# Kernel optimization log

Measured on AMD Instinct MI355X. Metric: run time of the kernel, lower is better.

## Reference

```python
import jax, jax.numpy as jnp
import numpy as np

TEMP = 10.0      # ZCA_temp -> diagonal regularizer 1/temp on the covariance
T_ITERS = 10     # ZCA_iteration: Newton-Schulz steps


def newton_zca(h, temp=TEMP, T=T_ITERS):
    """Newton-Schulz ZCA whitening of features h: [N, D].
    Returns (whitened [N,D], mean [1,D], whitening matrix C [D,D])."""
    n = h.shape[0]
    d = h.shape[1]
    mean = jnp.mean(h, axis=0, keepdims=True)            # [1, D]
    xc = h - mean                                        # [N, D]
    I = jnp.eye(d, dtype=h.dtype)
    cov = (xc.T @ xc) / n + I / temp                     # [D, D]
    tr = jnp.trace(cov)
    S = cov / tr                                         # spectral-normalized cov

    def step(P, _):
        # P <- 0.5 * (3 P - P^3 S)
        P = 1.5 * P - 0.5 * (P @ P @ (P @ S))
        return P, None

    P, _ = jax.lax.scan(step, I, None, length=T)
    C = P / jnp.sqrt(tr)                                 # cov^{-1/2}
    return xc @ C, mean, C


def setup_inputs() -> dict:
    key = jax.random.key(0)
    kx, k0, k1, k2 = jax.random.split(key, 4)
    N, DIN, D = 65536, 512, 512

    def glorot(k, din, dout):
        lim = jnp.sqrt(6.0 / (din + dout)).astype(jnp.float32)
        return jax.random.uniform(k, (din, dout), jnp.float32, -lim, lim)

    return {
        "x": jax.random.normal(kx, (N, DIN), jnp.float32),
        "W0": glorot(k0, DIN, D),
        "W1": glorot(k1, D, D),
        "W2": glorot(k2, D, D),
    }


def reference(x, W0, W1, W2):
    # training=True path, activation = identity, dropout rate 0.0 (identity).
    h0, _, _ = newton_zca(x @ W0)    # dense 0 + ZCA
    h1, _, _ = newton_zca(h0 @ W1)   # dense 1 + ZCA
    h2, _, _ = newton_zca(h1 @ W2)   # output dense + ZCA
    # deep_copy_list of per-layer activations
    return (h0, h1, h2)
```

## Files before the change

### kernel.cpp

```cpp
#include <hip/hip_runtime.h>

#define NROWS 65536
#define DIM   512
#define INV_N (1.0f/65536.0f)
#define INV_TEMP 0.1f
#define T_ITERS 10

__global__ __launch_bounds__(256) void colsum_part_k(const float* __restrict__ in,
                                                     float* __restrict__ part) {
    int ch = blockIdx.x;
    int t  = threadIdx.x;
    int c  = 2 * t;
    const float* p = in + (size_t)ch * 1024 * DIM + c;
    float s0 = 0.f, s1 = 0.f;
    for (int r = 0; r < 1024; ++r) {
        float2 v = *reinterpret_cast<const float2*>(p + (size_t)r * DIM);
        s0 += v.x; s1 += v.y;
    }
    part[ch * DIM + c]     = s0;
    part[ch * DIM + c + 1] = s1;
}

__global__ __launch_bounds__(256) void gram_k(const float* __restrict__ in,
                                              float* __restrict__ gp) {
    __shared__ float As[16][68];
    __shared__ float Bs[16][68];
    int ci0 = blockIdx.x * 64, cj0 = blockIdx.y * 64;
    int z = blockIdx.z;
    int t = threadIdx.x;
    int tx = t & 15, ty = t >> 4;
    int lr = t >> 4;
    int lc = (t & 15) * 4;
    float acc[4][4] = {};
    const float* baseA = in + (size_t)z * 4096 * DIM;
    const float* pa = baseA + (size_t)lr * DIM + ci0 + lc;
    const float* pb = baseA + (size_t)lr * DIM + cj0 + lc;
    float4 a = *reinterpret_cast<const float4*>(pa);
    float4 b = *reinterpret_cast<const float4*>(pb);
    for (int k0 = 0; k0 < 4096; k0 += 16) {
        __syncthreads();
        *reinterpret_cast<float4*>(&As[lr][lc]) = a;
        *reinterpret_cast<float4*>(&Bs[lr][lc]) = b;
        __syncthreads();
        if (k0 + 16 < 4096) {
            a = *reinterpret_cast<const float4*>(pa + (size_t)(k0 + 16) * DIM);
            b = *reinterpret_cast<const float4*>(pb + (size_t)(k0 + 16) * DIM);
        }
#pragma unroll
        for (int k = 0; k < 16; ++k) {
            float4 av = *reinterpret_cast<const float4*>(&As[k][4 * ty]);
            float4 bv = *reinterpret_cast<const float4*>(&Bs[k][4 * tx]);
            float aa[4] = {av.x, av.y, av.z, av.w};
            float bb[4] = {bv.x, bv.y, bv.z, bv.w};
#pragma unroll
            for (int i = 0; i < 4; ++i)
#pragma unroll
                for (int j = 0; j < 4; ++j)
                    acc[i][j] = fmaf(aa[i], bb[j], acc[i][j]);
        }
    }
    float* o = gp + (size_t)z * DIM * DIM;
#pragma unroll
    for (int i = 0; i < 4; ++i) {
        float4 v = {acc[i][0], acc[i][1], acc[i][2], acc[i][3]};
        *reinterpret_cast<float4*>(o + (size_t)(ci0 + 4 * ty + i) * DIM + cj0 + 4 * tx) = v;
    }
}

__global__ __launch_bounds__(256) void gram_reduce_k(const float* __restrict__ gp,
                                                     float* __restrict__ G) {
    int idx = (blockIdx.x * 256 + threadIdx.x) * 4;
    float4 s = {0.f, 0.f, 0.f, 0.f};
    for (int ch = 0; ch < 16; ++ch) {
        float4 v = *reinterpret_cast<const float4*>(gp + (size_t)ch * DIM * DIM + idx);
        s.x += v.x; s.y += v.y; s.z += v.z; s.w += v.w;
    }
    *reinterpret_cast<float4*>(G + idx) = s;
}

__global__ __launch_bounds__(256) void meanh_k(const float* __restrict__ part,
                                               const float* __restrict__ W,
                                               float* __restrict__ mh) {
    __shared__ float cs[DIM];
    int t = threadIdx.x;
    for (int c = t; c < DIM; c += 256) {
        float s = 0.f;
        for (int ch = 0; ch < 64; ++ch) s += part[ch * DIM + c];
        cs[c] = s;
    }
    __syncthreads();
    for (int c = t; c < DIM; c += 256) {
        float s = 0.f;
        for (int k = 0; k < DIM; ++k) s = fmaf(cs[k], W[(size_t)k * DIM + c], s);
        mh[c] = s * INV_N;
    }
}

__device__ __forceinline__ void small_gemm_body(const float* __restrict__ A, int ta,
                                                const float* __restrict__ B,
                                                float* __restrict__ C, int mode,
                                                const float* __restrict__ scal, int sidx,
                                                int bx, int by) {
    __shared__ float As[32][36];
    __shared__ float Bs[32][36];
    int m0 = bx * 32, n0 = by * 32;
    int t = threadIdx.x;
    int tx = t & 15, ty = t >> 4;
    int lr = t >> 3;
    int lc = (t & 7) * 4;
    float acc[2][2] = {};
    float4 av, bv;
    if (ta) av = *reinterpret_cast<const float4*>(A + (size_t)lr * DIM + m0 + lc);
    else    av = *reinterpret_cast<const float4*>(A + (size_t)(m0 + lr) * DIM + lc);
    bv = *reinterpret_cast<const float4*>(B + (size_t)lr * DIM + n0 + lc);
    for (int k0 = 0; k0 < DIM; k0 += 32) {
        __syncthreads();
        if (ta) {
            *reinterpret_cast<float4*>(&As[lr][lc]) = av;
        } else {
            As[lc + 0][lr] = av.x; As[lc + 1][lr] = av.y;
            As[lc + 2][lr] = av.z; As[lc + 3][lr] = av.w;
        }
        *reinterpret_cast<float4*>(&Bs[lr][lc]) = bv;
        __syncthreads();
        if (k0 + 32 < DIM) {
            if (ta) av = *reinterpret_cast<const float4*>(A + (size_t)(k0 + 32 + lr) * DIM + m0 + lc);
            else    av = *reinterpret_cast<const float4*>(A + (size_t)(m0 + lr) * DIM + k0 + 32 + lc);
            bv = *reinterpret_cast<const float4*>(B + (size_t)(k0 + 32 + lr) * DIM + n0 + lc);
        }
#pragma unroll
        for (int k = 0; k < 32; ++k) {
            float a0 = As[k][2 * ty], a1 = As[k][2 * ty + 1];
            float b0 = Bs[k][2 * tx], b1 = Bs[k][2 * tx + 1];
            acc[0][0] = fmaf(a0, b0, acc[0][0]);
            acc[0][1] = fmaf(a0, b1, acc[0][1]);
            acc[1][0] = fmaf(a1, b0, acc[1][0]);
            acc[1][1] = fmaf(a1, b1, acc[1][1]);
        }
    }
    int m = m0 + 2 * ty, nn = n0 + 2 * tx;
    size_t i00 = (size_t)m * DIM + nn, i10 = (size_t)(m + 1) * DIM + nn;
    if (mode == 0) {
        C[i00] = acc[0][0]; C[i00 + 1] = acc[0][1];
        C[i10] = acc[1][0]; C[i10 + 1] = acc[1][1];
    } else if (mode == 1) {
        C[i00]     = 1.5f * C[i00]     - 0.5f * acc[0][0];
        C[i00 + 1] = 1.5f * C[i00 + 1] - 0.5f * acc[0][1];
        C[i10]     = 1.5f * C[i10]     - 0.5f * acc[1][0];
        C[i10 + 1] = 1.5f * C[i10 + 1] - 0.5f * acc[1][1];
    } else {
        float s = scal[sidx];
        C[i00] = acc[0][0] * s; C[i00 + 1] = acc[0][1] * s;
        C[i10] = acc[1][0] * s; C[i10 + 1] = acc[1][1] * s;
    }
}

__global__ __launch_bounds__(256) void small_gemm_k(const float* __restrict__ A, int ta,
                                                    const float* __restrict__ B,
                                                    float* __restrict__ C, int mode,
                                                    const float* __restrict__ scal, int sidx) {
    small_gemm_body(A, ta, B, C, mode, scal, sidx, blockIdx.x, blockIdx.y);
}

__global__ __launch_bounds__(256) void ns_tt_k(const float* __restrict__ P,
                                               const float* __restrict__ S,
                                               float* __restrict__ T1,
                                               float* __restrict__ T2) {
    if (blockIdx.z == 0) small_gemm_body(P, 0, P, T1, 0, nullptr, 0, blockIdx.x, blockIdx.y);
    else                 small_gemm_body(P, 0, S, T2, 0, nullptr, 0, blockIdx.x, blockIdx.y);
}

__global__ __launch_bounds__(256) void trace_k(const float* __restrict__ covh,
                                               const float* __restrict__ mh,
                                               float* __restrict__ scal) {
    __shared__ float red[256];
    int t = threadIdx.x;
    float s = 0.f;
    for (int i = t; i < DIM; i += 256)
        s += covh[(size_t)i * DIM + i] * INV_N - mh[i] * mh[i] + INV_TEMP;
    red[t] = s;
    __syncthreads();
    for (int o = 128; o > 0; o >>= 1) {
        if (t < o) red[t] += red[t + o];
        __syncthreads();
    }
    if (t == 0) {
        float tr = red[0];
        scal[0] = 1.0f / tr;
        scal[1] = 1.0f / sqrtf(tr);
    }
}

__global__ __launch_bounds__(256) void makeS_k(const float* __restrict__ covh,
                                               const float* __restrict__ mh,
                                               const float* __restrict__ scal,
                                               float* __restrict__ S) {
    int idx = blockIdx.x * 256 + threadIdx.x;
    int i = idx >> 9, j = idx & 511;
    float v = covh[idx] * INV_N - mh[i] * mh[j] + ((i == j) ? INV_TEMP : 0.f);
    S[idx] = v * scal[0];
}

__global__ __launch_bounds__(256) void initP_k(float* __restrict__ P) {
    int idx = blockIdx.x * 256 + threadIdx.x;
    int i = idx >> 9, j = idx & 511;
    P[idx] = (i == j) ? 1.0f : 0.f;
}

__global__ __launch_bounds__(256) void bias_k(const float* __restrict__ mh,
                                              const float* __restrict__ P,
                                              const float* __restrict__ scal,
                                              float* __restrict__ bias) {
    __shared__ float m_s[DIM];
    int t = threadIdx.x;
    for (int c = t; c < DIM; c += 256) m_s[c] = mh[c];
    __syncthreads();
    float ist = scal[1];
    for (int c = t; c < DIM; c += 256) {
        float s = 0.f;
        for (int k = 0; k < DIM; ++k) s = fmaf(m_s[k], P[(size_t)k * DIM + c], s);
        bias[c] = s * ist;
    }
}

__global__ __launch_bounds__(256) void out_gemm_k(const float* __restrict__ in,
                                                  const float* __restrict__ WC,
                                                  const float* __restrict__ bias,
                                                  float* __restrict__ out) {
    __shared__ float As[16][68];
    __shared__ float Bs[16][68];
    int n0 = blockIdx.x * 64, m0 = blockIdx.y * 64;
    int t = threadIdx.x;
    int tx = t & 15, ty = t >> 4;
    int ar = t >> 2;
    int ac = (t & 3) * 4;
    int br = t >> 4;
    int bc = (t & 15) * 4;
    float acc[4][4] = {};
    const float* pa = in + (size_t)(m0 + ar) * DIM + ac;
    const float* pb = WC + (size_t)br * DIM + n0 + bc;
    float4 a = *reinterpret_cast<const float4*>(pa);
    float4 b = *reinterpret_cast<const float4*>(pb);
    for (int k0 = 0; k0 < DIM; k0 += 16) {
        __syncthreads();
        As[ac + 0][ar] = a.x; As[ac + 1][ar] = a.y;
        As[ac + 2][ar] = a.z; As[ac + 3][ar] = a.w;
        *reinterpret_cast<float4*>(&Bs[br][bc]) = b;
        __syncthreads();
        if (k0 + 16 < DIM) {
            a = *reinterpret_cast<const float4*>(pa + k0 + 16);
            b = *reinterpret_cast<const float4*>(pb + (size_t)(k0 + 16) * DIM);
        }
#pragma unroll
        for (int k = 0; k < 16; ++k) {
            float4 av = *reinterpret_cast<const float4*>(&As[k][4 * ty]);
            float4 bv = *reinterpret_cast<const float4*>(&Bs[k][4 * tx]);
            float aa[4] = {av.x, av.y, av.z, av.w};
            float bb[4] = {bv.x, bv.y, bv.z, bv.w};
#pragma unroll
            for (int i = 0; i < 4; ++i)
#pragma unroll
                for (int j = 0; j < 4; ++j)
                    acc[i][j] = fmaf(aa[i], bb[j], acc[i][j]);
        }
    }
    float4 bvv = *reinterpret_cast<const float4*>(bias + n0 + 4 * tx);
    float bb[4] = {bvv.x, bvv.y, bvv.z, bvv.w};
#pragma unroll
    for (int i = 0; i < 4; ++i) {
        float4 v = {acc[i][0] - bb[0], acc[i][1] - bb[1],
                    acc[i][2] - bb[2], acc[i][3] - bb[3]};
        *reinterpret_cast<float4*>(out + (size_t)(m0 + 4 * ty + i) * DIM + n0 + 4 * tx) = v;
    }
}

extern "C" void kernel_launch(void* const* d_in, const int* in_sizes, int n_in,
                              void* d_out, int out_size, void* d_ws, size_t ws_size,
                              hipStream_t stream) {
    const float* x = (const float*)d_in[0];
    const float* Wl[3] = {(const float*)d_in[1], (const float*)d_in[2], (const float*)d_in[3]};
    float* out = (float*)d_out;
    float* ws  = (float*)d_ws;

    const size_t MM = (size_t)DIM * DIM;
    float* G     = ws;
    float* S     = G + MM;
    float* P     = S + MM;
    float* T1    = P + MM;
    float* T2    = T1 + MM;
    float* covh  = T2 + MM;
    float* WC    = covh + MM;
    float* gramp = WC + MM;
    float* cpart = gramp + 16 * MM;
    float* mh    = cpart + 64 * DIM;
    float* bias  = mh + DIM;
    float* scal  = bias + DIM;

    for (int l = 0; l < 3; ++l) {
        const float* in = (l == 0) ? x : out + (size_t)(l - 1) * NROWS * DIM;
        const float* W  = Wl[l];
        float* o = out + (size_t)l * NROWS * DIM;

        colsum_part_k<<<64, 256, 0, stream>>>(in, cpart);
        gram_k<<<dim3(8, 8, 16), 256, 0, stream>>>(in, gramp);
        gram_reduce_k<<<256, 256, 0, stream>>>(gramp, G);
        meanh_k<<<1, 256, 0, stream>>>(cpart, W, mh);
        small_gemm_k<<<dim3(16, 16), 256, 0, stream>>>(G, 0, W, T1, 0, nullptr, 0);
        small_gemm_k<<<dim3(16, 16), 256, 0, stream>>>(W, 1, T1, covh, 0, nullptr, 0);
        trace_k<<<1, 256, 0, stream>>>(covh, mh, scal);
        makeS_k<<<1024, 256, 0, stream>>>(covh, mh, scal, S);
        initP_k<<<1024, 256, 0, stream>>>(P);
        for (int it = 0; it < T_ITERS; ++it) {
            ns_tt_k<<<dim3(16, 16, 2), 256, 0, stream>>>(P, S, T1, T2);
            small_gemm_k<<<dim3(16, 16), 256, 0, stream>>>(T1, 0, T2, P, 1, nullptr, 0);
        }
        small_gemm_k<<<dim3(16, 16), 256, 0, stream>>>(W, 0, P, WC, 2, scal, 1);
        bias_k<<<1, 256, 0, stream>>>(mh, P, scal, bias);
        out_gemm_k<<<dim3(8, 1024), 256, 0, stream>>>(in, WC, bias, o);
    }
}
```

Baseline: 4.952 ms.

## Rewrite ZCA pipeline with split-bf16 MFMA gemms and cooperative Newton-Schulz kernel

The Gram matrix and output GEMMs now run on MFMA bf16 instructions with a hi/lo split (three products) to approximate fp32 accuracy. The Gram is computed only for upper-triangular tiles, accumulated with atomics, and fused with the column sum. The small-matrix chain (covariance, trace, Newton-Schulz iterations, WC and bias) moves into one cooperative kernel with grid syncs instead of dozens of launches, with a multi-kernel fallback. The costs are reduced precision from the bf16 split, atomic contention, and dependence on cooperative launch support.

```diff
diff --git a/kernel.cpp b/kernel.cpp
--- a/kernel.cpp
+++ b/kernel.cpp
@@ -1,4 +1,7 @@
 #include <hip/hip_runtime.h>
+#include <hip/hip_cooperative_groups.h>
+
+namespace cg = cooperative_groups;
 
 #define NROWS 65536
 #define DIM   512
@@ -6,113 +9,162 @@
 #define INV_TEMP 0.1f
 #define T_ITERS 10
 
-__global__ __launch_bounds__(256) void colsum_part_k(const float* __restrict__ in,
-                                                     float* __restrict__ part) {
-    int ch = blockIdx.x;
-    int t  = threadIdx.x;
-    int c  = 2 * t;
-    const float* p = in + (size_t)ch * 1024 * DIM + c;
-    float s0 = 0.f, s1 = 0.f;
-    for (int r = 0; r < 1024; ++r) {
-        float2 v = *reinterpret_cast<const float2*>(p + (size_t)r * DIM);
-        s0 += v.x; s1 += v.y;
-    }
-    part[ch * DIM + c]     = s0;
-    part[ch * DIM + c + 1] = s1;
-}
-
-__global__ __launch_bounds__(256) void gram_k(const float* __restrict__ in,
-                                              float* __restrict__ gp) {
-    __shared__ float As[16][68];
-    __shared__ float Bs[16][68];
-    int ci0 = blockIdx.x * 64, cj0 = blockIdx.y * 64;
-    int z = blockIdx.z;
+typedef __attribute__((ext_vector_type(8))) short bf16x8;
+typedef __attribute__((ext_vector_type(4))) float f32x4;
+
+#define OFF_G    0
+#define OFF_SCAL 262144
+#define OFF_CS   262208
+#define OFF_S    262720
+#define OFF_P    (OFF_S  + 262144)
+#define OFF_T1   (OFF_P  + 262144)
+#define OFF_T2   (OFF_T1 + 262144)
+#define OFF_CV   (OFF_T2 + 262144)
+#define OFF_MH   (OFF_CV + 262144)
+#define OFF_BIAS (OFF_MH + 512)
+#define OFF_WCH  (OFF_BIAS + 512)
+#define OFF_WCL  (OFF_WCH + 131072)
+
+__device__ __forceinline__ unsigned short bf_hi(float x) {
+    return (unsigned short)(__float_as_uint(x) >> 16);
+}
+__device__ __forceinline__ float bf_f(unsigned short h) {
+    return __uint_as_float(((unsigned)h) << 16);
+}
+
+__global__ __launch_bounds__(256) void zero_k(float* __restrict__ ws) {
+    int idx = blockIdx.x * 256 + threadIdx.x;
+    if (idx < 65680) reinterpret_cast<float4*>(ws)[idx] = make_float4(0.f, 0.f, 0.f, 0.f);
+}
+
+__global__ __launch_bounds__(256, 2) void gram_k(const float* __restrict__ in,
+                                                 float* __restrict__ G,
+                                                 float* __restrict__ cs) {
+    __shared__ unsigned short Ah[128][40], Al[128][40], Bh[128][40], Bl[128][40];
+    int u = blockIdx.x, z = blockIdx.y;
+    int bi, bj;
+    if (u < 4)      { bi = 0; bj = u; }
+    else if (u < 7) { bi = 1; bj = u - 3; }
+    else if (u < 9) { bi = 2; bj = u - 5; }
+    else            { bi = 3; bj = 3; }
+    bool diag = (bi == bj);
+    int ci0 = bi * 128, cj0 = bj * 128;
+    int t = threadIdx.x;
+    int d = t & 127, nh = (t >> 7) * 16;
+    const float* baseA = in + (size_t)z * 2048 * DIM + ci0 + d;
+    const float* baseB = in + (size_t)z * 2048 * DIM + cj0 + d;
+    int lane = t & 63, w = t >> 6;
+    int wr = (w >> 1) * 64, wc = (w & 1) * 64;
+    int fr = lane & 15, kg = lane >> 4;
+    f32x4 acc[4][4];
+#pragma unroll
+    for (int i = 0; i < 4; ++i)
+#pragma unroll
+        for (int j = 0; j < 4; ++j) acc[i][j] = (f32x4){0.f, 0.f, 0.f, 0.f};
+    float pA[16], pB[16];
+    float csum = 0.f;
+#pragma unroll
+    for (int j = 0; j < 16; ++j) pA[j] = baseA[(size_t)(nh + j) * DIM];
+    if (!diag) {
+#pragma unroll
+        for (int j = 0; j < 16; ++j) pB[j] = baseB[(size_t)(nh + j) * DIM];
+    }
+    for (int s = 0; s < 64; ++s) {
+        __syncthreads();
+        if (diag) {
+#pragma unroll
+            for (int j = 0; j < 16; ++j) csum += pA[j];
+        }
+#pragma unroll
+        for (int gq = 0; gq < 2; ++gq) {
+            unsigned hw[4], lw[4];
+#pragma unroll
+            for (int q = 0; q < 4; ++q) {
+                float x0 = pA[gq * 8 + 2 * q], x1 = pA[gq * 8 + 2 * q + 1];
+                unsigned short h0 = bf_hi(x0), h1 = bf_hi(x1);
+                unsigned short l0 = bf_hi(x0 - bf_f(h0)), l1 = bf_hi(x1 - bf_f(h1));
+                hw[q] = (unsigned)h0 | ((unsigned)h1 << 16);
+                lw[q] = (unsigned)l0 | ((unsigned)l1 << 16);
+            }
+            *reinterpret_cast<uint4*>(&Ah[d][nh + 8 * gq]) = make_uint4(hw[0], hw[1], hw[2], hw[3]);
+            *reinterpret_cast<uint4*>(&Al[d][nh + 8 * gq]) = make_uint4(lw[0], lw[1], lw[2], lw[3]);
+        }
+        if (!diag) {
+#pragma unroll
+            for (int gq = 0; gq < 2; ++gq) {
+                unsigned hw[4], lw[4];
+#pragma unroll
+                for (int q = 0; q < 4; ++q) {
+                    float x0 = pB[gq * 8 + 2 * q], x1 = pB[gq * 8 + 2 * q + 1];
+                    unsigned short h0 = bf_hi(x0), h1 = bf_hi(x1);
+                    unsigned short l0 = bf_hi(x0 - bf_f(h0)), l1 = bf_hi(x1 - bf_f(h1));
+                    hw[q] = (unsigned)h0 | ((unsigned)h1 << 16);
+                    lw[q] = (unsigned)l0 | ((unsigned)l1 << 16);
+                }
+                *reinterpret_cast<uint4*>(&Bh[d][nh + 8 * gq]) = make_uint4(hw[0], hw[1], hw[2], hw[3]);
+                *reinterpret_cast<uint4*>(&Bl[d][nh + 8 * gq]) = make_uint4(lw[0], lw[1], lw[2], lw[3]);
+            }
+        }
+        __syncthreads();
+        if (s + 1 < 64) {
+#pragma unroll
+            for (int j = 0; j < 16; ++j)
+                pA[j] = baseA[(size_t)((s + 1) * 32 + nh + j) * DIM];
+            if (!diag) {
+#pragma unroll
+                for (int j = 0; j < 16; ++j)
+                    pB[j] = baseB[(size_t)((s + 1) * 32 + nh + j) * DIM];
+            }
+        }
+        const unsigned short (*pBh)[40] = diag ? Ah : Bh;
+        const unsigned short (*pBl)[40] = diag ? Al : Bl;
+        bf16x8 ah[4], al4[4], bh4[4], bl4[4];
+#pragma unroll
+        for (int f = 0; f < 4; ++f) {
+            ah[f]  = *reinterpret_cast<const bf16x8*>(&Ah[wr + f * 16 + fr][kg * 8]);
+            al4[f] = *reinterpret_cast<const bf16x8*>(&Al[wr + f * 16 + fr][kg * 8]);
+            bh4[f] = *reinterpret_cast<const bf16x8*>(&pBh[wc + f * 16 + fr][kg * 8]);
+            bl4[f] = *reinterpret_cast<const bf16x8*>(&pBl[wc + f * 16 + fr][kg * 8]);
+        }
+#pragma unroll
+        for (int i = 0; i < 4; ++i)
+#pragma unroll
+            for (int j = 0; j < 4; ++j) {
+                f32x4 c = acc[i][j];
+                c = __builtin_amdgcn_mfma_f32_16x16x32_bf16(ah[i],  bh4[j], c, 0, 0, 0);
+                c = __builtin_amdgcn_mfma_f32_16x16x32_bf16(ah[i],  bl4[j], c, 0, 0, 0);
+                c = __builtin_amdgcn_mfma_f32_16x16x32_bf16(al4[i], bh4[j], c, 0, 0, 0);
+                acc[i][j] = c;
+            }
+    }
+#pragma unroll
+    for (int i = 0; i < 4; ++i) {
+        int row = ci0 + wr + i * 16 + kg * 4;
+#pragma unroll
+        for (int j = 0; j < 4; ++j) {
+            int col = cj0 + wc + j * 16 + fr;
+#pragma unroll
+            for (int r = 0; r < 4; ++r)
+                atomicAdd(&G[(size_t)(row + r) * DIM + col], acc[i][j][r]);
+        }
+    }
+    if (diag) atomicAdd(&cs[ci0 + d], csum);
+}
+
+__device__ void gemm_tile(const float* __restrict__ A, int ta,
+                          const float* __restrict__ B,
+                          float* C, int tile, int mode, float* ws) {
+    __shared__ float As[32][36];
+    __shared__ float Bs[32][36];
+    int m0 = (tile >> 4) * 32, n0 = (tile & 15) * 32;
     int t = threadIdx.x;
     int tx = t & 15, ty = t >> 4;
-    int lr = t >> 4;
-    int lc = (t & 15) * 4;
-    float acc[4][4] = {};
-    const float* baseA = in + (size_t)z * 4096 * DIM;
-    const float* pa = baseA + (size_t)lr * DIM + ci0 + lc;
-    const float* pb = baseA + (size_t)lr * DIM + cj0 + lc;
-    float4 a = *reinterpret_cast<const float4*>(pa);
-    float4 b = *reinterpret_cast<const float4*>(pb);
-    for (int k0 = 0; k0 < 4096; k0 += 16) {
-        __syncthreads();
-        *reinterpret_cast<float4*>(&As[lr][lc]) = a;
-        *reinterpret_cast<float4*>(&Bs[lr][lc]) = b;
-        __syncthreads();
-        if (k0 + 16 < 4096) {
-            a = *reinterpret_cast<const float4*>(pa + (size_t)(k0 + 16) * DIM);
-            b = *reinterpret_cast<const float4*>(pb + (size_t)(k0 + 16) * DIM);
-        }
-#pragma unroll
-        for (int k = 0; k < 16; ++k) {
-            float4 av = *reinterpret_cast<const float4*>(&As[k][4 * ty]);
-            float4 bv = *reinterpret_cast<const float4*>(&Bs[k][4 * tx]);
-            float aa[4] = {av.x, av.y, av.z, av.w};
-            float bb[4] = {bv.x, bv.y, bv.z, bv.w};
-#pragma unroll
-            for (int i = 0; i < 4; ++i)
-#pragma unroll
-                for (int j = 0; j < 4; ++j)
-                    acc[i][j] = fmaf(aa[i], bb[j], acc[i][j]);
-        }
-    }
-    float* o = gp + (size_t)z * DIM * DIM;
-#pragma unroll
-    for (int i = 0; i < 4; ++i) {
-        float4 v = {acc[i][0], acc[i][1], acc[i][2], acc[i][3]};
-        *reinterpret_cast<float4*>(o + (size_t)(ci0 + 4 * ty + i) * DIM + cj0 + 4 * tx) = v;
-    }
-}
-
-__global__ __launch_bounds__(256) void gram_reduce_k(const float* __restrict__ gp,
-                                                     float* __restrict__ G) {
-    int idx = (blockIdx.x * 256 + threadIdx.x) * 4;
-    float4 s = {0.f, 0.f, 0.f, 0.f};
-    for (int ch = 0; ch < 16; ++ch) {
-        float4 v = *reinterpret_cast<const float4*>(gp + (size_t)ch * DIM * DIM + idx);
-        s.x += v.x; s.y += v.y; s.z += v.z; s.w += v.w;
-    }
-    *reinterpret_cast<float4*>(G + idx) = s;
-}
-
-__global__ __launch_bounds__(256) void meanh_k(const float* __restrict__ part,
-                                               const float* __restrict__ W,
-                                               float* __restrict__ mh) {
-    __shared__ float cs[DIM];
-    int t = threadIdx.x;
-    for (int c = t; c < DIM; c += 256) {
-        float s = 0.f;
-        for (int ch = 0; ch < 64; ++ch) s += part[ch * DIM + c];
-        cs[c] = s;
-    }
-    __syncthreads();
-    for (int c = t; c < DIM; c += 256) {
-        float s = 0.f;
-        for (int k = 0; k < DIM; ++k) s = fmaf(cs[k], W[(size_t)k * DIM + c], s);
-        mh[c] = s * INV_N;
-    }
-}
-
-__device__ __forceinline__ void small_gemm_body(const float* __restrict__ A, int ta,
-                                                const float* __restrict__ B,
-                                                float* __restrict__ C, int mode,
-                                                const float* __restrict__ scal, int sidx,
-                                                int bx, int by) {
-    __shared__ float As[32][36];
-    __shared__ float Bs[32][36];
-    int m0 = bx * 32, n0 = by * 32;
-    int t = threadIdx.x;
-    int tx = t & 15, ty = t >> 4;
-    int lr = t >> 3;
-    int lc = (t & 7) * 4;
-    float acc[2][2] = {};
+    int lr = t >> 3, lc = (t & 7) * 4;
+    float acc00 = 0.f, acc01 = 0.f, acc10 = 0.f, acc11 = 0.f;
     float4 av, bv;
-    if (ta) av = *reinterpret_cast<const float4*>(A + (size_t)lr * DIM + m0 + lc);
-    else    av = *reinterpret_cast<const float4*>(A + (size_t)(m0 + lr) * DIM + lc);
-    bv = *reinterpret_cast<const float4*>(B + (size_t)lr * DIM + n0 + lc);
+    av = ta ? *reinterpret_cast<const float4*>(&A[(size_t)lr * DIM + m0 + lc])
+            : *reinterpret_cast<const float4*>(&A[(size_t)(m0 + lr) * DIM + lc]);
+    bv = *reinterpret_cast<const float4*>(&B[(size_t)lr * DIM + n0 + lc]);
     for (int k0 = 0; k0 < DIM; k0 += 32) {
         __syncthreads();
         if (ta) {
@@ -124,198 +176,299 @@
         *reinterpret_cast<float4*>(&Bs[lr][lc]) = bv;
         __syncthreads();
         if (k0 + 32 < DIM) {
-            if (ta) av = *reinterpret_cast<const float4*>(A + (size_t)(k0 + 32 + lr) * DIM + m0 + lc);
-            else    av = *reinterpret_cast<const float4*>(A + (size_t)(m0 + lr) * DIM + k0 + 32 + lc);
-            bv = *reinterpret_cast<const float4*>(B + (size_t)(k0 + 32 + lr) * DIM + n0 + lc);
+            av = ta ? *reinterpret_cast<const float4*>(&A[(size_t)(k0 + 32 + lr) * DIM + m0 + lc])
+                    : *reinterpret_cast<const float4*>(&A[(size_t)(m0 + lr) * DIM + k0 + 32 + lc]);
+            bv = *reinterpret_cast<const float4*>(&B[(size_t)(k0 + 32 + lr) * DIM + n0 + lc]);
         }
 #pragma unroll
         for (int k = 0; k < 32; ++k) {
             float a0 = As[k][2 * ty], a1 = As[k][2 * ty + 1];
             float b0 = Bs[k][2 * tx], b1 = Bs[k][2 * tx + 1];
-            acc[0][0] = fmaf(a0, b0, acc[0][0]);
-            acc[0][1] = fmaf(a0, b1, acc[0][1]);
-            acc[1][0] = fmaf(a1, b0, acc[1][0]);
-            acc[1][1] = fmaf(a1, b1, acc[1][1]);
-        }
-    }
-    int m = m0 + 2 * ty, nn = n0 + 2 * tx;
-    size_t i00 = (size_t)m * DIM + nn, i10 = (size_t)(m + 1) * DIM + nn;
+            acc00 = fmaf(a0, b0, acc00); acc01 = fmaf(a0, b1, acc01);
+            acc10 = fmaf(a1, b0, acc10); acc11 = fmaf(a1, b1, acc11);
+        }
+    }
+    int m = m0 + 2 * ty, n = n0 + 2 * tx;
+    size_t i00 = (size_t)m * DIM + n, i10 = (size_t)(m + 1) * DIM + n;
     if (mode == 0) {
-        C[i00] = acc[0][0]; C[i00 + 1] = acc[0][1];
-        C[i10] = acc[1][0]; C[i10 + 1] = acc[1][1];
+        C[i00] = acc00; C[i00 + 1] = acc01; C[i10] = acc10; C[i10 + 1] = acc11;
     } else if (mode == 1) {
-        C[i00]     = 1.5f * C[i00]     - 0.5f * acc[0][0];
-        C[i00 + 1] = 1.5f * C[i00 + 1] - 0.5f * acc[0][1];
-        C[i10]     = 1.5f * C[i10]     - 0.5f * acc[1][0];
-        C[i10 + 1] = 1.5f * C[i10 + 1] - 0.5f * acc[1][1];
+        C[i00]     = 1.5f * C[i00]     - 0.5f * acc00;
+        C[i00 + 1] = 1.5f * C[i00 + 1] - 0.5f * acc01;
+        C[i10]     = 1.5f * C[i10]     - 0.5f * acc10;
+        C[i10 + 1] = 1.5f * C[i10 + 1] - 0.5f * acc11;
+    } else if (mode == 2) {
+        C[i00] = acc00; C[i00 + 1] = acc01; C[i10] = acc10; C[i10 + 1] = acc11;
+        if (m == n) atomicAdd(ws + OFF_SCAL, (acc00 + acc11) * INV_N);
     } else {
-        float s = scal[sidx];
-        C[i00] = acc[0][0] * s; C[i00 + 1] = acc[0][1] * s;
-        C[i10] = acc[1][0] * s; C[i10 + 1] = acc[1][1] * s;
-    }
-}
-
-__global__ __launch_bounds__(256) void small_gemm_k(const float* __restrict__ A, int ta,
-                                                    const float* __restrict__ B,
-                                                    float* __restrict__ C, int mode,
-                                                    const float* __restrict__ scal, int sidx) {
-    small_gemm_body(A, ta, B, C, mode, scal, sidx, blockIdx.x, blockIdx.y);
-}
-
-__global__ __launch_bounds__(256) void ns_tt_k(const float* __restrict__ P,
-                                               const float* __restrict__ S,
-                                               float* __restrict__ T1,
-                                               float* __restrict__ T2) {
-    if (blockIdx.z == 0) small_gemm_body(P, 0, P, T1, 0, nullptr, 0, blockIdx.x, blockIdx.y);
-    else                 small_gemm_body(P, 0, S, T2, 0, nullptr, 0, blockIdx.x, blockIdx.y);
-}
-
-__global__ __launch_bounds__(256) void trace_k(const float* __restrict__ covh,
-                                               const float* __restrict__ mh,
-                                               float* __restrict__ scal) {
+        unsigned short* WCth = (unsigned short*)(ws + OFF_WCH);
+        unsigned short* WCtl = (unsigned short*)(ws + OFF_WCL);
+        float istr = 1.0f / sqrtf(ws[OFF_SCAL]);
+        float v;
+        unsigned short h;
+        v = acc00 * istr; h = bf_hi(v);
+        WCth[(size_t)n * DIM + m] = h;           WCtl[(size_t)n * DIM + m] = bf_hi(v - bf_f(h));
+        v = acc01 * istr; h = bf_hi(v);
+        WCth[(size_t)(n + 1) * DIM + m] = h;     WCtl[(size_t)(n + 1) * DIM + m] = bf_hi(v - bf_f(h));
+        v = acc10 * istr; h = bf_hi(v);
+        WCth[(size_t)n * DIM + m + 1] = h;       WCtl[(size_t)n * DIM + m + 1] = bf_hi(v - bf_f(h));
+        v = acc11 * istr; h = bf_hi(v);
+        WCth[(size_t)(n + 1) * DIM + m + 1] = h; WCtl[(size_t)(n + 1) * DIM + m + 1] = bf_hi(v - bf_f(h));
+    }
+}
+
+__global__ __launch_bounds__(256) void coop_k(float* ws, const float* __restrict__ W) {
+    cg::grid_group g = cg::this_grid();
+    float* G  = ws + OFF_G;   float* scal = ws + OFF_SCAL;
+    float* cs = ws + OFF_CS;  float* S    = ws + OFF_S;
+    float* P  = ws + OFF_P;   float* T1   = ws + OFF_T1;
+    float* T2 = ws + OFF_T2;  float* CV   = ws + OFF_CV;
+    float* mh = ws + OFF_MH;  float* bias = ws + OFF_BIAS;
+    int b = blockIdx.x, t = threadIdx.x;
+    int gtid = b * 256 + t;
+#pragma unroll
+    for (int e = 0; e < 4; ++e) {
+        int idx = gtid * 4 + e;
+        int i = idx >> 9, j = idx & 511;
+        if (i < j) G[(size_t)j * DIM + i] = G[idx];
+    }
+    g.sync();
+    gemm_tile(G, 0, W, T1, b, 0, ws);
+    if (b == 0) {
+        for (int c = t; c < DIM; c += 256) {
+            float s = 0.f;
+            for (int k = 0; k < DIM; ++k) s = fmaf(cs[k], W[(size_t)k * DIM + c], s);
+            mh[c] = s * INV_N;
+        }
+    }
+    g.sync();
+    gemm_tile(W, 1, T1, CV, b, 2, ws);
+    if (b == 0) {
+        __shared__ float red[256];
+        red[t] = mh[t] * mh[t] + mh[t + 256] * mh[t + 256];
+        __syncthreads();
+        for (int o = 128; o > 0; o >>= 1) { if (t < o) red[t] += red[t + o]; __syncthreads(); }
+        if (t == 0) atomicAdd(scal, 51.2f - red[0]);
+    }
+    g.sync();
+    {
+        float invtr = 1.0f / scal[0];
+#pragma unroll
+        for (int e = 0; e < 4; ++e) {
+            int idx = gtid * 4 + e;
+            int i = idx >> 9, j = idx & 511;
+            float v = CV[idx] * INV_N - mh[i] * mh[j] + ((i == j) ? INV_TEMP : 0.f);
+            S[idx] = v * invtr;
+            P[idx] = (i == j) ? 1.f : 0.f;
+        }
+    }
+    g.sync();
+    for (int it = 0; it < T_ITERS; ++it) {
+        gemm_tile(P, 0, P, T1, b, 0, ws);
+        gemm_tile(P, 0, S, T2, b, 0, ws);
+        g.sync();
+        gemm_tile(T1, 0, T2, P, b, 1, ws);
+        g.sync();
+    }
+    gemm_tile(W, 0, P, nullptr, b, 3, ws);
+    if (b == 0) {
+        float istr = 1.0f / sqrtf(scal[0]);
+        for (int c = t; c < DIM; c += 256) {
+            float s = 0.f;
+            for (int k = 0; k < DIM; ++k) s = fmaf(mh[k], P[(size_t)k * DIM + c], s);
+            bias[c] = s * istr;
+        }
+    }
+}
+
+__global__ __launch_bounds__(256, 2) void out_k(const float* __restrict__ in,
+                                                const unsigned short* __restrict__ WCth,
+                                                const unsigned short* __restrict__ WCtl,
+                                                const float* __restrict__ bias,
+                                                float* __restrict__ out) {
+    __shared__ unsigned short Ah[128][72], Al[128][72], Bh[128][72], Bl[128][72];
+    int n0 = blockIdx.x * 128, m0 = blockIdx.y * 128;
+    int t = threadIdx.x;
+    int lane = t & 63, w = t >> 6;
+    int wr = (w >> 1) * 64, wc = (w & 1) * 64;
+    int fr = lane & 15, kg = lane >> 4;
+    int am = t >> 4, aq = (t & 15) * 4;
+    int bn = t >> 3, bc = (t & 7) * 8;
+    f32x4 acc[4][4];
+#pragma unroll
+    for (int i = 0; i < 4; ++i)
+#pragma unroll
+        for (int j = 0; j < 4; ++j) acc[i][j] = (f32x4){0.f, 0.f, 0.f, 0.f};
+    float4 pa[8]; uint4 pbh[4], pbl[4];
+#pragma unroll
+    for (int p = 0; p < 8; ++p)
+        pa[p] = *reinterpret_cast<const float4*>(&in[(size_t)(m0 + p * 16 + am) * DIM + aq]);
+#pragma unroll
+    for (int p = 0; p < 4; ++p) {
+        pbh[p] = *reinterpret_cast<const uint4*>(&WCth[(size_t)(n0 + p * 32 + bn) * DIM + bc]);
+        pbl[p] = *reinterpret_cast<const uint4*>(&WCtl[(size_t)(n0 + p * 32 + bn) * DIM + bc]);
+    }
+    for (int s = 0; s < 8; ++s) {
+        __syncthreads();
+#pragma unroll
+        for (int p = 0; p < 8; ++p) {
+            float4 v = pa[p];
+            unsigned short h0 = bf_hi(v.x), h1 = bf_hi(v.y), h2 = bf_hi(v.z), h3 = bf_hi(v.w);
+            unsigned short l0 = bf_hi(v.x - bf_f(h0)), l1 = bf_hi(v.y - bf_f(h1));
+            unsigned short l2 = bf_hi(v.z - bf_f(h2)), l3 = bf_hi(v.w - bf_f(h3));
+            *reinterpret_cast<uint2*>(&Ah[p * 16 + am][aq]) =
+                make_uint2((unsigned)h0 | ((unsigned)h1 << 16), (unsigned)h2 | ((unsigned)h3 << 16));
+            *reinterpret_cast<uint2*>(&Al[p * 16 + am][aq]) =
+                make_uint2((unsigned)l0 | ((unsigned)l1 << 16), (unsigned)l2 | ((unsigned)l3 << 16));
+        }
+#pragma unroll
+        for (int p = 0; p < 4; ++p) {
+            *reinterpret_cast<uint4*>(&Bh[p * 32 + bn][bc]) = pbh[p];
+            *reinterpret_cast<uint4*>(&Bl[p * 32 + bn][bc]) = pbl[p];
+        }
+        __syncthreads();
+        if (s + 1 < 8) {
+            int k0 = (s + 1) * 64;
+#pragma unroll
+            for (int p = 0; p < 8; ++p)
+                pa[p] = *reinterpret_cast<const float4*>(&in[(size_t)(m0 + p * 16 + am) * DIM + k0 + aq]);
+#pragma unroll
+            for (int p = 0; p < 4; ++p) {
+                pbh[p] = *reinterpret_cast<const uint4*>(&WCth[(size_t)(n0 + p * 32 + bn) * DIM + k0 + bc]);
+                pbl[p] = *reinterpret_cast<const uint4*>(&WCtl[(size_t)(n0 + p * 32 + bn) * DIM + k0 + bc]);
+            }
+        }
+#pragma unroll
+        for (int k2 = 0; k2 < 2; ++k2) {
+            int ko = k2 * 32 + kg * 8;
+            bf16x8 ah[4], al4[4], bh4[4], bl4[4];
+#pragma unroll
+            for (int f = 0; f < 4; ++f) {
+                ah[f]  = *reinterpret_cast<const bf16x8*>(&Ah[wr + f * 16 + fr][ko]);
+                al4[f] = *reinterpret_cast<const bf16x8*>(&Al[wr + f * 16 + fr][ko]);
+                bh4[f] = *reinterpret_cast<const bf16x8*>(&Bh[wc + f * 16 + fr][ko]);
+                bl4[f] = *reinterpret_cast<const bf16x8*>(&Bl[wc + f * 16 + fr][ko]);
+            }
+#pragma unroll
+            for (int i = 0; i < 4; ++i)
+#pragma unroll
+                for (int j = 0; j < 4; ++j) {
+                    f32x4 c = acc[i][j];
+                    c = __builtin_amdgcn_mfma_f32_16x16x32_bf16(ah[i],  bh4[j], c, 0, 0, 0);
+                    c = __builtin_amdgcn_mfma_f32_16x16x32_bf16(ah[i],  bl4[j], c, 0, 0, 0);
+                    c = __builtin_amdgcn_mfma_f32_16x16x32_bf16(al4[i], bh4[j], c, 0, 0, 0);
+                    acc[i][j] = c;
+                }
+        }
+    }
+#pragma unroll
+    for (int j = 0; j < 4; ++j) {
+        int col = n0 + wc + j * 16 + fr;
+        float bb = bias[col];
+#pragma unroll
+        for (int i = 0; i < 4; ++i) {
+            int row = m0 + wr + i * 16 + kg * 4;
+#pragma unroll
+            for (int r = 0; r < 4; ++r)
+                out[(size_t)(row + r) * DIM + col] = acc[i][j][r] - bb;
+        }
+    }
+}
+
+__global__ __launch_bounds__(256) void tile_gemm_k(const float* __restrict__ A, int ta,
+                                                   const float* __restrict__ B,
+                                                   float* C, int mode, float* ws) {
+    gemm_tile(A, ta, B, C, blockIdx.x, mode, ws);
+}
+__global__ __launch_bounds__(256) void mirror_k(float* ws) {
+    float* G = ws + OFF_G;
+    int gtid = blockIdx.x * 256 + threadIdx.x;
+#pragma unroll
+    for (int e = 0; e < 4; ++e) {
+        int idx = gtid * 4 + e;
+        int i = idx >> 9, j = idx & 511;
+        if (i < j) G[(size_t)j * DIM + i] = G[idx];
+    }
+}
+__global__ __launch_bounds__(256) void mh_k(float* ws, const float* __restrict__ W) {
+    float* cs = ws + OFF_CS; float* mh = ws + OFF_MH;
+    int c = blockIdx.x * 256 + threadIdx.x;
+    float s = 0.f;
+    for (int k = 0; k < DIM; ++k) s = fmaf(cs[k], W[(size_t)k * DIM + c], s);
+    mh[c] = s * INV_N;
+}
+__global__ __launch_bounds__(256) void trmh_k(float* ws) {
     __shared__ float red[256];
+    float* mh = ws + OFF_MH;
     int t = threadIdx.x;
+    red[t] = mh[t] * mh[t] + mh[t + 256] * mh[t + 256];
+    __syncthreads();
+    for (int o = 128; o > 0; o >>= 1) { if (t < o) red[t] += red[t + o]; __syncthreads(); }
+    if (t == 0) atomicAdd(ws + OFF_SCAL, 51.2f - red[0]);
+}
+__global__ __launch_bounds__(256) void makeSP_k(float* ws) {
+    float* CV = ws + OFF_CV; float* mh = ws + OFF_MH;
+    float* S = ws + OFF_S;   float* P = ws + OFF_P;
+    float invtr = 1.0f / ws[OFF_SCAL];
+    int gtid = blockIdx.x * 256 + threadIdx.x;
+#pragma unroll
+    for (int e = 0; e < 4; ++e) {
+        int idx = gtid * 4 + e;
+        int i = idx >> 9, j = idx & 511;
+        float v = CV[idx] * INV_N - mh[i] * mh[j] + ((i == j) ? INV_TEMP : 0.f);
+        S[idx] = v * invtr;
+        P[idx] = (i == j) ? 1.f : 0.f;
+    }
+}
+__global__ __launch_bounds__(256) void bias_k(float* ws) {
+    float* mh = ws + OFF_MH; float* P = ws + OFF_P; float* bias = ws + OFF_BIAS;
+    float istr = 1.0f / sqrtf(ws[OFF_SCAL]);
+    int c = blockIdx.x * 256 + threadIdx.x;
     float s = 0.f;
-    for (int i = t; i < DIM; i += 256)
-        s += covh[(size_t)i * DIM + i] * INV_N - mh[i] * mh[i] + INV_TEMP;
-    red[t] = s;
-    __syncthreads();
-    for (int o = 128; o > 0; o >>= 1) {
-        if (t < o) red[t] += red[t + o];
-        __syncthreads();
-    }
-    if (t == 0) {
-        float tr = red[0];
-        scal[0] = 1.0f / tr;
-        scal[1] = 1.0f / sqrtf(tr);
-    }
-}
-
-__global__ __launch_bounds__(256) void makeS_k(const float* __restrict__ covh,
-                                               const float* __restrict__ mh,
-                                               const float* __restrict__ scal,
-                                               float* __restrict__ S) {
-    int idx = blockIdx.x * 256 + threadIdx.x;
-    int i = idx >> 9, j = idx & 511;
-    float v = covh[idx] * INV_N - mh[i] * mh[j] + ((i == j) ? INV_TEMP : 0.f);
-    S[idx] = v * scal[0];
-}
-
-__global__ __launch_bounds__(256) void initP_k(float* __restrict__ P) {
-    int idx = blockIdx.x * 256 + threadIdx.x;
-    int i = idx >> 9, j = idx & 511;
-    P[idx] = (i == j) ? 1.0f : 0.f;
-}
-
-__global__ __launch_bounds__(256) void bias_k(const float* __restrict__ mh,
-                                              const float* __restrict__ P,
-                                              const float* __restrict__ scal,
-                                              float* __restrict__ bias) {
-    __shared__ float m_s[DIM];
-    int t = threadIdx.x;
-    for (int c = t; c < DIM; c += 256) m_s[c] = mh[c];
-    __syncthreads();
-    float ist = scal[1];
-    for (int c = t; c < DIM; c += 256) {
-        float s = 0.f;
-        for (int k = 0; k < DIM; ++k) s = fmaf(m_s[k], P[(size_t)k * DIM + c], s);
-        bias[c] = s * ist;
-    }
-}
-
-__global__ __launch_bounds__(256) void out_gemm_k(const float* __restrict__ in,
-                                                  const float* __restrict__ WC,
-                                                  const float* __restrict__ bias,
-                                                  float* __restrict__ out) {
-    __shared__ float As[16][68];
-    __shared__ float Bs[16][68];
-    int n0 = blockIdx.x * 64, m0 = blockIdx.y * 64;
-    int t = threadIdx.x;
-    int tx = t & 15, ty = t >> 4;
-    int ar = t >> 2;
-    int ac = (t & 3) * 4;
-    int br = t >> 4;
-    int bc = (t & 15) * 4;
-    float acc[4][4] = {};
-    const float* pa = in + (size_t)(m0 + ar) * DIM + ac;
-    const float* pb = WC + (size_t)br * DIM + n0 + bc;
-    float4 a = *reinterpret_cast<const float4*>(pa);
-    float4 b = *reinterpret_cast<const float4*>(pb);
-    for (int k0 = 0; k0 < DIM; k0 += 16) {
-        __syncthreads();
-        As[ac + 0][ar] = a.x; As[ac + 1][ar] = a.y;
-        As[ac + 2][ar] = a.z; As[ac + 3][ar] = a.w;
-        *reinterpret_cast<float4*>(&Bs[br][bc]) = b;
-        __syncthreads();
-        if (k0 + 16 < DIM) {
-            a = *reinterpret_cast<const float4*>(pa + k0 + 16);
-            b = *reinterpret_cast<const float4*>(pb + (size_t)(k0 + 16) * DIM);
-        }
-#pragma unroll
-        for (int k = 0; k < 16; ++k) {
-            float4 av = *reinterpret_cast<const float4*>(&As[k][4 * ty]);
-            float4 bv = *reinterpret_cast<const float4*>(&Bs[k][4 * tx]);
-            float aa[4] = {av.x, av.y, av.z, av.w};
-            float bb[4] = {bv.x, bv.y, bv.z, bv.w};
-#pragma unroll
-            for (int i = 0; i < 4; ++i)
-#pragma unroll
-                for (int j = 0; j < 4; ++j)
-                    acc[i][j] = fmaf(aa[i], bb[j], acc[i][j]);
-        }
-    }
-    float4 bvv = *reinterpret_cast<const float4*>(bias + n0 + 4 * tx);
-    float bb[4] = {bvv.x, bvv.y, bvv.z, bvv.w};
-#pragma unroll
-    for (int i = 0; i < 4; ++i) {
-        float4 v = {acc[i][0] - bb[0], acc[i][1] - bb[1],
-                    acc[i][2] - bb[2], acc[i][3] - bb[3]};
-        *reinterpret_cast<float4*>(out + (size_t)(m0 + 4 * ty + i) * DIM + n0 + 4 * tx) = v;
-    }
+    for (int k = 0; k < DIM; ++k) s = fmaf(mh[k], P[(size_t)k * DIM + c], s);
+    bias[c] = s * istr;
 }
 
 extern "C" void kernel_launch(void* const* d_in, const int* in_sizes, int n_in,
                               void* d_out, int out_size, void* d_ws, size_t ws_size,
                               hipStream_t stream) {
+    (void)in_sizes; (void)n_in; (void)out_size; (void)ws_size;
     const float* x = (const float*)d_in[0];
     const float* Wl[3] = {(const float*)d_in[1], (const float*)d_in[2], (const float*)d_in[3]};
     float* out = (float*)d_out;
     float* ws  = (float*)d_ws;
 
-    const size_t MM = (size_t)DIM * DIM;
-    float* G     = ws;
-    float* S     = G + MM;
-    float* P     = S + MM;
-    float* T1    = P + MM;
-    float* T2    = T1 + MM;
-    float* covh  = T2 + MM;
-    float* WC    = covh + MM;
-    float* gramp = WC + MM;
-    float* cpart = gramp + 16 * MM;
-    float* mh    = cpart + 64 * DIM;
-    float* bias  = mh + DIM;
-    float* scal  = bias + DIM;
-
     for (int l = 0; l < 3; ++l) {
         const float* in = (l == 0) ? x : out + (size_t)(l - 1) * NROWS * DIM;
         const float* W  = Wl[l];
         float* o = out + (size_t)l * NROWS * DIM;
 
-        colsum_part_k<<<64, 256, 0, stream>>>(in, cpart);
-        gram_k<<<dim3(8, 8, 16), 256, 0, stream>>>(in, gramp);
-        gram_reduce_k<<<256, 256, 0, stream>>>(gramp, G);
-        meanh_k<<<1, 256, 0, stream>>>(cpart, W, mh);
-        small_gemm_k<<<dim3(16, 16), 256, 0, stream>>>(G, 0, W, T1, 0, nullptr, 0);
-        small_gemm_k<<<dim3(16, 16), 256, 0, stream>>>(W, 1, T1, covh, 0, nullptr, 0);
-        trace_k<<<1, 256, 0, stream>>>(covh, mh, scal);
-        makeS_k<<<1024, 256, 0, stream>>>(covh, mh, scal, S);
-        initP_k<<<1024, 256, 0, stream>>>(P);
-        for (int it = 0; it < T_ITERS; ++it) {
-            ns_tt_k<<<dim3(16, 16, 2), 256, 0, stream>>>(P, S, T1, T2);
-            small_gemm_k<<<dim3(16, 16), 256, 0, stream>>>(T1, 0, T2, P, 1, nullptr, 0);
-        }
-        small_gemm_k<<<dim3(16, 16), 256, 0, stream>>>(W, 0, P, WC, 2, scal, 1);
-        bias_k<<<1, 256, 0, stream>>>(mh, P, scal, bias);
-        out_gemm_k<<<dim3(8, 1024), 256, 0, stream>>>(in, WC, bias, o);
-    }
-}
+        zero_k<<<257, 256, 0, stream>>>(ws);
+        gram_k<<<dim3(10, 32), 256, 0, stream>>>(in, ws + OFF_G, ws + OFF_CS);
+
+        float* wsp = ws;
+        const float* wp = W;
+        void* cargs[2] = {(void*)&wsp, (void*)&wp};
+        hipError_t ce = hipLaunchCooperativeKernel((void*)coop_k, dim3(256), dim3(256),
+                                                   cargs, 0, stream);
+        if (ce != hipSuccess) {
+            mirror_k<<<256, 256, 0, stream>>>(ws);
+            tile_gemm_k<<<256, 256, 0, stream>>>(ws + OFF_G, 0, W, ws + OFF_T1, 0, ws);
+            mh_k<<<2, 256, 0, stream>>>(ws, W);
+            tile_gemm_k<<<256, 256, 0, stream>>>(W, 1, ws + OFF_T1, ws + OFF_CV, 2, ws);
+            trmh_k<<<1, 256, 0, stream>>>(ws);
+            makeSP_k<<<256, 256, 0, stream>>>(ws);
+            for (int it = 0; it < T_ITERS; ++it) {
+                tile_gemm_k<<<256, 256, 0, stream>>>(ws + OFF_P, 0, ws + OFF_P, ws + OFF_T1, 0, ws);
+                tile_gemm_k<<<256, 256, 0, stream>>>(ws + OFF_P, 0, ws + OFF_S, ws + OFF_T2, 0, ws);
+                tile_gemm_k<<<256, 256, 0, stream>>>(ws + OFF_T1, 0, ws + OFF_T2, ws + OFF_P, 1, ws);
+            }
+            tile_gemm_k<<<256, 256, 0, stream>>>(W, 0, ws + OFF_P, nullptr, 3, ws);
+            bias_k<<<2, 256, 0, stream>>>(ws);
+        }
+
+        out_k<<<dim3(4, 512), 256, 0, stream>>>(in,
+            (const unsigned short*)(ws + OFF_WCH), (const unsigned short*)(ws + OFF_WCL),
+            ws + OFF_BIAS, o);
+    }
+}
```

New measurement: 4.966 ms. Within noise of the previous version (+0.3%).
